# Kernel tuning notes

Measured on AMD Instinct MI355X. Metric: run time of the kernel, lower is better.

Reference implementation:

```python
import jax, jax.numpy as jnp
import numpy as np

WS = 7          # window size
SIZE = 56       # spatial H = W
SHIFT = 3       # shift_size = window_size // 2 (mask branch active)
NH = 4          # num heads
EPS = 1e-5


def _rel_pos_index(ws=WS):
    coords = np.stack(np.meshgrid(np.arange(ws), np.arange(ws), indexing='ij'))  # [2,ws,ws]
    coords = coords.reshape(2, -1)                               # [2, ws*ws]
    rel = coords[:, :, None] - coords[:, None, :]                # [2, N, N]
    rel = rel.transpose(1, 2, 0)                                 # [N, N, 2]
    rel[:, :, 0] += ws - 1
    rel[:, :, 1] += ws - 1
    rel[:, :, 0] *= 2 * ws - 1
    return jnp.asarray(rel[:, :, 0] + rel[:, :, 1])              # [N, N] int


def _attn_mask(size=SIZE, ws=WS, shift=SHIFT):
    img = np.zeros((size, size), dtype=np.float32)
    slices = (slice(0, -ws), slice(-ws, -shift), slice(-shift, None))
    cnt = 0
    for h in slices:
        for w in slices:
            img[h, w] = cnt
            cnt += 1
    nw = size // ws
    win = img.reshape(nw, ws, nw, ws).transpose(0, 2, 1, 3).reshape(-1, ws * ws)  # [nW, N]
    diff = win[:, None, :] - win[:, :, None]                    # [nW, N, N]
    mask = np.where(diff != 0, -100.0, 0.0).astype(np.float32)
    return jnp.asarray(mask)


def _layernorm(x, w, b):
    mu = jnp.mean(x, axis=-1, keepdims=True)
    var = jnp.mean(jnp.square(x - mu), axis=-1, keepdims=True)
    return (x - mu) * jax.lax.rsqrt(var + EPS) * w + b


def setup_inputs() -> dict:
    key = jax.random.key(0)
    ks = jax.random.split(key, 8)
    dim, dff = 128, 512
    s = lambda fan: 1.0 / np.sqrt(fan)
    return {
        'x': jax.random.normal(ks[0], (32, SIZE * SIZE, dim), jnp.float32),
        'qkv_w': jax.random.normal(ks[1], (dim, 3 * dim), jnp.float32) * s(dim),
        'qkv_b': jnp.zeros((3 * dim,), jnp.float32),
        'proj_w': jax.random.normal(ks[2], (dim, dim), jnp.float32) * s(dim),
        'proj_b': jnp.zeros((dim,), jnp.float32),
        'rpb_table': jax.random.normal(ks[3], ((2 * WS - 1) ** 2, NH), jnp.float32) * 0.02,
        'ln1_w': jnp.ones((dim,), jnp.float32),
        'ln1_b': jnp.zeros((dim,), jnp.float32),
        'ln2_w': jnp.ones((dim,), jnp.float32),
        'ln2_b': jnp.zeros((dim,), jnp.float32),
        'mlp_w1': jax.random.normal(ks[4], (dim, dff), jnp.float32) * s(dim),
        'mlp_b1': jnp.zeros((dff,), jnp.float32),
        'mlp_w2': jax.random.normal(ks[5], (dff, dim), jnp.float32) * s(dff),
        'mlp_b2': jnp.zeros((dim,), jnp.float32),
    }


def reference(x, qkv_w, qkv_b, proj_w, proj_b, rpb_table,
              ln1_w, ln1_b, ln2_w, ln2_b, mlp_w1, mlp_b1, mlp_w2, mlp_b2):
    B, L, C = x.shape
    N = WS * WS
    nw = SIZE // WS
    nW = nw * nw
    hd = C // NH
    scale = hd ** -0.5

    shortcut = x
    h = _layernorm(x, ln1_w, ln1_b).reshape(B, SIZE, SIZE, C)
    # window partition -> [B*nW, N, C]
    h = h.reshape(B, nw, WS, nw, WS, C).transpose(0, 1, 3, 2, 4, 5).reshape(B * nW, N, C)

    qkv = (h @ qkv_w + qkv_b).reshape(B * nW, N, 3, NH, hd)
    q, k, v = jnp.moveaxis(qkv, 2, 0)                 # each [B*nW, N, NH, hd]
    attn = jnp.einsum('bnhd,bmhd->bhnm', q * scale, k)  # [B*nW, NH, N, N]

    bias = rpb_table[_rel_pos_index()]                # [N, N, NH]
    attn = attn + bias.transpose(2, 0, 1)[None]

    mask = _attn_mask()                               # [nW, N, N]
    attn = attn.reshape(B, nW, NH, N, N) + mask[None, :, None]
    attn = jax.nn.softmax(attn.reshape(B * nW, NH, N, N), axis=-1)

    h = jnp.einsum('bhnm,bmhd->bnhd', attn, v).reshape(B * nW, N, C)
    h = h @ proj_w + proj_b

    # window reverse -> [B, L, C]
    h = h.reshape(B, nw, nw, WS, WS, C).transpose(0, 1, 3, 2, 4, 5).reshape(B, L, C)
    x = shortcut + h

    m = _layernorm(x, ln2_w, ln2_b)
    m = jax.nn.gelu(m @ mlp_w1 + mlp_b1, approximate=False) @ mlp_w2 + mlp_b2
    return x + m
```

## Files before the change

kernel.cpp:

```cpp
#include <hip/hip_runtime.h>
#include <hip/hip_bf16.h>

#define T_TOK   100352
#define NWIN    2048
#define EPS_LN  1e-5f

typedef __attribute__((ext_vector_type(8))) short bf16x8;
typedef __attribute__((ext_vector_type(4))) float f32x4;

__device__ inline unsigned short f2bf(float f) {
  union { float f; unsigned int i; } c; c.f = f;
  unsigned int x = c.i;
  x += 0x7fffu + ((x >> 16) & 1u);
  return (unsigned short)(x >> 16);
}
__device__ inline bf16x8 ld8(const unsigned short* p) {
  return *reinterpret_cast<const bf16x8*>(p);
}

__device__ inline int win_row_to_token(int r) {
  int win = r / 49, n = r % 49;
  int b  = win >> 6, w2 = win & 63;
  int wi = w2 >> 3,  wj = w2 & 7;
  int rr = n / 7,    cc = n % 7;
  return b * 3136 + (wi * 7 + rr) * 56 + (wj * 7 + cc);
}

__global__ void prep_weights(const float* __restrict__ qkv_w,
                             const float* __restrict__ proj_w,
                             const float* __restrict__ w1,
                             const float* __restrict__ w2,
                             unsigned short* __restrict__ wts) {
  int i = blockIdx.x * 256 + threadIdx.x;
  unsigned short* qkvt  = wts;
  unsigned short* projt = wts + 49152;
  unsigned short* w1t   = wts + 65536;
  unsigned short* w2t   = wts + 131072;
  if (i < 49152) {
    int n = i >> 7, k = i & 127; qkvt[i] = f2bf(qkv_w[k * 384 + n]);
  } else if (i < 65536) {
    int e = i - 49152; int n = e >> 7, k = e & 127; projt[e] = f2bf(proj_w[k * 128 + n]);
  } else if (i < 131072) {
    int e = i - 65536; int n = e >> 7, k = e & 127; w1t[e] = f2bf(w1[k * 512 + n]);
  } else if (i < 196608) {
    int e = i - 131072; int n = e >> 9, k = e & 511; w2t[e] = f2bf(w2[k * 128 + n]);
  }
}

__global__ void prep_cls(const float* __restrict__ rpb, float* __restrict__ cls2) {
  int i = blockIdx.x * 256 + threadIdx.x;
  int reg = i & 3, lane = (i >> 2) & 63, ct = (i >> 8) & 3, rt = (i >> 10) & 3,
      h = (i >> 12) & 3, cl = (i >> 14) & 3;
  int n = rt * 16 + ((lane >> 4) << 2) + reg;
  int m = ct * 16 + (lane & 15);
  float v = -30000.f;
  if (n < 49 && m < 49) {
    int nr = n / 7, nc = n % 7, mr = m / 7, mc = m % 7;
    v = rpb[((nr - mr + 6) * 13 + (nc - mc + 6)) * 4 + h];
    int regn = ((cl & 2) ? (nr < 4 ? 3 : 6) : 0) + ((cl & 1) ? (nc < 4 ? 1 : 2) : 0);
    int regm = ((cl & 2) ? (mr < 4 ? 3 : 6) : 0) + ((cl & 1) ? (mc < 4 ? 1 : 2) : 0);
    if (regn != regm) v -= 100.f;
  }
  cls2[i] = v;
}

template<bool WINMAP>
__global__ __launch_bounds__(256) void ln_kernel(const float* __restrict__ x,
                                                 const float* __restrict__ w,
                                                 const float* __restrict__ b,
                                                 unsigned short* __restrict__ out) {
  int r    = blockIdx.x * 4 + (threadIdx.x >> 6);
  int lane = threadIdx.x & 63;
  int src  = WINMAP ? win_row_to_token(r) : r;
  float2 v = *reinterpret_cast<const float2*>(x + (long)src * 128 + lane * 2);
  float s  = v.x + v.y;
  float s2 = v.x * v.x + v.y * v.y;
#pragma unroll
  for (int off = 32; off; off >>= 1) {
    s  += __shfl_xor(s,  off);
    s2 += __shfl_xor(s2, off);
  }
  float mu  = s * (1.f / 128.f);
  float var = s2 * (1.f / 128.f) - mu * mu;
  float inv = rsqrtf(var + EPS_LN);
  int c = lane * 2;
  float2 wv = *reinterpret_cast<const float2*>(w + c);
  float2 bv = *reinterpret_cast<const float2*>(b + c);
  float y0 = (v.x - mu) * inv * wv.x + bv.x;
  float y1 = (v.y - mu) * inv * wv.y + bv.y;
  unsigned int pk = ((unsigned int)f2bf(y1) << 16) | (unsigned int)f2bf(y0);
  *reinterpret_cast<unsigned int*>(out + (long)r * 128 + c) = pk;
}

template<int EPI, int KSTEPS, int NBN>
__global__ __launch_bounds__(256) void gemm_k(const unsigned short* __restrict__ A,
                                              const unsigned short* __restrict__ Wt,
                                              const float* __restrict__ bias,
                                              void* __restrict__ out,
                                              const float* __restrict__ res) {
  const int K = KSTEPS * 32;
  int flat  = blockIdx.x;
  int chunk = gridDim.x >> 3;
  int swz   = (flat & 7) * chunk + (flat >> 3);
  int ntile = swz % NBN, mpan = swz / NBN;

  int lane = threadIdx.x & 63;
  int wid  = threadIdx.x >> 6;
  int rowBase = mpan * 128 + wid * 32;
  int colBase = ntile * 64;
  int m  = lane & 15;
  int kg = lane >> 4;
  f32x4 acc[2][4] = {};
  const unsigned short* Ap = A  + (long)(rowBase + m) * K + kg * 8;
  const unsigned short* Bp = Wt + (long)(colBase + m) * K + kg * 8;
#pragma unroll 4
  for (int ks = 0; ks < KSTEPS; ks++) {
    bf16x8 b0 = ld8(Bp + 0 * 16 * K + ks * 32);
    bf16x8 b1 = ld8(Bp + 1 * 16 * K + ks * 32);
    bf16x8 b2 = ld8(Bp + 2 * 16 * K + ks * 32);
    bf16x8 b3 = ld8(Bp + 3 * 16 * K + ks * 32);
    bf16x8 a0 = ld8(Ap + ks * 32);
    bf16x8 a1 = ld8(Ap + (long)16 * K + ks * 32);
    acc[0][0] = __builtin_amdgcn_mfma_f32_16x16x32_bf16(a0, b0, acc[0][0], 0, 0, 0);
    acc[0][1] = __builtin_amdgcn_mfma_f32_16x16x32_bf16(a0, b1, acc[0][1], 0, 0, 0);
    acc[0][2] = __builtin_amdgcn_mfma_f32_16x16x32_bf16(a0, b2, acc[0][2], 0, 0, 0);
    acc[0][3] = __builtin_amdgcn_mfma_f32_16x16x32_bf16(a0, b3, acc[0][3], 0, 0, 0);
    acc[1][0] = __builtin_amdgcn_mfma_f32_16x16x32_bf16(a1, b0, acc[1][0], 0, 0, 0);
    acc[1][1] = __builtin_amdgcn_mfma_f32_16x16x32_bf16(a1, b1, acc[1][1], 0, 0, 0);
    acc[1][2] = __builtin_amdgcn_mfma_f32_16x16x32_bf16(a1, b2, acc[1][2], 0, 0, 0);
    acc[1][3] = __builtin_amdgcn_mfma_f32_16x16x32_bf16(a1, b3, acc[1][3], 0, 0, 0);
  }
#pragma unroll
  for (int mt = 0; mt < 2; mt++) {
#pragma unroll
    for (int rgi = 0; rgi < 4; rgi++) {
      int row = rowBase + mt * 16 + kg * 4 + rgi;
      int t = (EPI == 1) ? win_row_to_token(row) : row;
#pragma unroll
      for (int j = 0; j < 4; j++) {
        int col = colBase + j * 16 + m;
        float v = acc[mt][j][rgi] + bias[col];
        if (EPI == 0) {
          ((unsigned short*)out)[(long)row * 384 + col] = f2bf(v);
        } else {
          ((float*)out)[(long)t * 128 + col] = res[(long)t * 128 + col] + v;
        }
      }
    }
  }
}

__global__ __launch_bounds__(256) void attn_mfma(const unsigned short* __restrict__ qkv,
                                                 const float* __restrict__ cls2,
                                                 unsigned short* __restrict__ out) {
  __shared__ unsigned short vt[128 * 64];
  __shared__ unsigned short pb[4][64 * 64];
  int win = blockIdx.x;
  int tid = threadIdx.x;
  const unsigned short* qbase = qkv + (long)win * 49 * 384;

  for (int i = tid; i < 49 * 128; i += 256) {
    int mm = i >> 7, d = i & 127;
    vt[d * 64 + (mm ^ ((d & 7) << 3))] = qbase[mm * 384 + 256 + d];
  }
  for (int i = tid; i < 128 * 15; i += 256) {
    int d = i / 15, mm = 49 + i % 15;
    vt[d * 64 + (mm ^ ((d & 7) << 3))] = 0;
  }

  int h = tid >> 6, lane = tid & 63;
  int lr = lane & 15, g = lane >> 4;
  int w2 = win & 63;
  int cl = (((w2 >> 3) == 7) ? 2 : 0) + (((w2 & 7) == 7) ? 1 : 0);

  bf16x8 aq[4], bk[4];
  bf16x8 zf = {};
#pragma unroll
  for (int rt = 0; rt < 4; rt++)
    aq[rt] = ld8(qbase + (rt * 16 + lr) * 384 + h * 32 + g * 8);
#pragma unroll
  for (int ct = 0; ct < 4; ct++) {
    int mm = ct * 16 + lr;
    bk[ct] = (mm < 49) ? ld8(qbase + mm * 384 + 128 + h * 32 + g * 8) : zf;
  }
  f32x4 acc[4][4] = {};
#pragma unroll
  for (int rt = 0; rt < 4; rt++)
#pragma unroll
    for (int ct = 0; ct < 4; ct++)
      acc[rt][ct] = __builtin_amdgcn_mfma_f32_16x16x32_bf16(aq[rt], bk[ct], acc[rt][ct], 0, 0, 0);

  const float scale = 0.17677669529663687f;
  const float* cb = cls2 + (long)(cl * 4 + h) * 16 * 256;
  unsigned short* P = pb[h];
#pragma unroll
  for (int rt = 0; rt < 4; rt++) {
    f32x4 c[4];
#pragma unroll
    for (int ct = 0; ct < 4; ct++)
      c[ct] = *reinterpret_cast<const f32x4*>(cb + (rt * 4 + ct) * 256 + lane * 4);
#pragma unroll
    for (int reg = 0; reg < 4; reg++) {
      float s0 = acc[rt][0][reg] * scale + c[0][reg];
      float s1 = acc[rt][1][reg] * scale + c[1][reg];
      float s2 = acc[rt][2][reg] * scale + c[2][reg];
      float s3 = acc[rt][3][reg] * scale + c[3][reg];
      float mx = fmaxf(fmaxf(s0, s1), fmaxf(s2, s3));
      mx = fmaxf(mx, __shfl_xor(mx, 1)); mx = fmaxf(mx, __shfl_xor(mx, 2));
      mx = fmaxf(mx, __shfl_xor(mx, 4)); mx = fmaxf(mx, __shfl_xor(mx, 8));
      float p0 = __expf(s0 - mx), p1 = __expf(s1 - mx);
      float p2 = __expf(s2 - mx), p3 = __expf(s3 - mx);
      float sum = p0 + p1 + p2 + p3;
      sum += __shfl_xor(sum, 1); sum += __shfl_xor(sum, 2);
      sum += __shfl_xor(sum, 4); sum += __shfl_xor(sum, 8);
      float inv = 1.f / sum;
      int n = rt * 16 + g * 4 + reg;
      int sw = (n & 7) << 3, rowb = n * 64;
      P[rowb + ((0 * 16 + lr) ^ sw)] = f2bf(p0 * inv);
      P[rowb + ((1 * 16 + lr) ^ sw)] = f2bf(p1 * inv);
      P[rowb + ((2 * 16 + lr) ^ sw)] = f2bf(p2 * inv);
      P[rowb + ((3 * 16 + lr) ^ sw)] = f2bf(p3 * inv);
    }
  }
  __syncthreads();

  f32x4 o[4][2] = {};
  bf16x8 bv[2][2];
#pragma unroll
  for (int dt = 0; dt < 2; dt++)
#pragma unroll
    for (int ks = 0; ks < 2; ks++) {
      int d = h * 32 + dt * 16 + lr;
      bv[dt][ks] = ld8(&vt[d * 64 + ((ks * 32 + g * 8) ^ ((d & 7) << 3))]);
    }
#pragma unroll
  for (int rt = 0; rt < 4; rt++)
#pragma unroll
    for (int ks = 0; ks < 2; ks++) {
      int n = rt * 16 + lr;
      bf16x8 ap = ld8(&P[n * 64 + ((ks * 32 + g * 8) ^ ((n & 7) << 3))]);
#pragma unroll
      for (int dt = 0; dt < 2; dt++)
        o[rt][dt] = __builtin_amdgcn_mfma_f32_16x16x32_bf16(ap, bv[dt][ks], o[rt][dt], 0, 0, 0);
    }
#pragma unroll
  for (int rt = 0; rt < 4; rt++)
#pragma unroll
    for (int dt = 0; dt < 2; dt++)
#pragma unroll
      for (int reg = 0; reg < 4; reg++) {
        int n = rt * 16 + g * 4 + reg;
        if (n < 49)
          out[((long)win * 49 + n) * 128 + h * 32 + dt * 16 + lr] = f2bf(o[rt][dt][reg]);
      }
}

__global__ __launch_bounds__(512, 1) void mlp_fused(
    const float* __restrict__ out1,
    const unsigned short* __restrict__ w1t,
    const float* __restrict__ b1,
    const unsigned short* __restrict__ w2t,
    const float* __restrict__ b2,
    const float* __restrict__ ln2w,
    const float* __restrict__ ln2b,
    float* __restrict__ dout) {
  __shared__ unsigned short lnm[64 * 136];
  __shared__ unsigned short gel[64 * 520];
  long rowbase = (long)blockIdx.x * 64;
  int tid = threadIdx.x, w = tid >> 6, lane = tid & 63, lr = lane & 15, g = lane >> 4;

  {
    int c = lane * 2;
    float2 wv = *(const float2*)(ln2w + c);
    float2 bv = *(const float2*)(ln2b + c);
    for (int n = w; n < 64; n += 8) {
      float2 v = *(const float2*)(out1 + (rowbase + n) * 128 + c);
      float s = v.x + v.y, s2 = v.x * v.x + v.y * v.y;
#pragma unroll
      for (int off = 32; off; off >>= 1) { s += __shfl_xor(s, off); s2 += __shfl_xor(s2, off); }
      float mu  = s * (1.f / 128.f);
      float inv = rsqrtf(s2 * (1.f / 128.f) - mu * mu + EPS_LN);
      float y0 = (v.x - mu) * inv * wv.x + bv.x;
      float y1 = (v.y - mu) * inv * wv.y + bv.y;
      unsigned int pk = ((unsigned int)f2bf(y1) << 16) | f2bf(y0);
      *(unsigned int*)(lnm + n * 136 + c) = pk;
    }
  }
  __syncthreads();

  f32x4 acc[4][4] = {};
#pragma unroll
  for (int ksi = 0; ksi < 4; ksi++) {
    int kof = ksi * 32 + g * 8;
    bf16x8 av[4], bv[4];
#pragma unroll
    for (int rt = 0; rt < 4; rt++)
      av[rt] = ld8(lnm + (rt * 16 + lr) * 136 + kof);
#pragma unroll
    for (int ct = 0; ct < 4; ct++) {
      int colc = w * 64 + ct * 16 + lr;
      bv[ct] = ld8(w1t + colc * 128 + kof);
    }
#pragma unroll
    for (int rt = 0; rt < 4; rt++)
#pragma unroll
      for (int ct = 0; ct < 4; ct++)
        acc[rt][ct] = __builtin_amdgcn_mfma_f32_16x16x32_bf16(av[rt], bv[ct], acc[rt][ct], 0, 0, 0);
  }
#pragma unroll
  for (int ct = 0; ct < 4; ct++) {
    int c = w * 64 + ct * 16 + lr;
    float bc = b1[c];
#pragma unroll
    for (int rt = 0; rt < 4; rt++)
#pragma unroll
      for (int rgi = 0; rgi < 4; rgi++) {
        int n = rt * 16 + g * 4 + rgi;
        float v = acc[rt][ct][rgi] + bc;
        float u = v * (1.0f + 0.044715f * v * v);
        float gv = v / (1.0f + __expf(-1.5957691216f * u));
        gel[n * 520 + c] = f2bf(gv);
      }
  }
  __syncthreads();

  f32x4 a2[4] = {};
#pragma unroll 4
  for (int ksi = 0; ksi < 16; ksi++) {
    int kof = ksi * 32 + g * 8;
    bf16x8 aa[4];
#pragma unroll
    for (int rt = 0; rt < 4; rt++)
      aa[rt] = ld8(gel + (rt * 16 + lr) * 520 + kof);
    bf16x8 bb = ld8(w2t + (w * 16 + lr) * 512 + kof);
#pragma unroll
    for (int rt = 0; rt < 4; rt++)
      a2[rt] = __builtin_amdgcn_mfma_f32_16x16x32_bf16(aa[rt], bb, a2[rt], 0, 0, 0);
  }
  int col = w * 16 + lr;
  float bc2 = b2[col];
#pragma unroll
  for (int rt = 0; rt < 4; rt++)
#pragma unroll
    for (int rgi = 0; rgi < 4; rgi++) {
      long row = rowbase + rt * 16 + g * 4 + rgi;
      dout[row * 128 + col] = out1[row * 128 + col] + bc2 + a2[rt][rgi];
    }
}

extern "C" void kernel_launch(void* const* d_in, const int* in_sizes, int n_in,
                              void* d_out, int out_size, void* d_ws, size_t ws_size,
                              hipStream_t stream) {
  (void)in_sizes; (void)n_in; (void)out_size; (void)ws_size;
  const float* x      = (const float*)d_in[0];
  const float* qkv_w  = (const float*)d_in[1];
  const float* qkv_b  = (const float*)d_in[2];
  const float* proj_w = (const float*)d_in[3];
  const float* proj_b = (const float*)d_in[4];
  const float* rpb    = (const float*)d_in[5];
  const float* ln1_w  = (const float*)d_in[6];
  const float* ln1_b  = (const float*)d_in[7];
  const float* ln2_w  = (const float*)d_in[8];
  const float* ln2_b  = (const float*)d_in[9];
  const float* w1     = (const float*)d_in[10];
  const float* b1     = (const float*)d_in[11];
  const float* w2     = (const float*)d_in[12];
  const float* b2     = (const float*)d_in[13];

  char* ws = (char*)d_ws;
  unsigned short* wts   = (unsigned short*)ws;
  unsigned short* hb    = (unsigned short*)(ws + 393216);
  unsigned short* qkv   = (unsigned short*)(ws + 26083328);
  unsigned short* attno = hb;
  float*          out1  = (float*)(ws + 103153664);
  float*          cls2  = (float*)(ws + 154533888);

  const int MP = T_TOK / 128;

  prep_weights<<<768, 256, 0, stream>>>(qkv_w, proj_w, w1, w2, wts);
  prep_cls<<<256, 256, 0, stream>>>(rpb, cls2);
  ln_kernel<true><<<T_TOK / 4, 256, 0, stream>>>(x, ln1_w, ln1_b, hb);
  gemm_k<0, 4, 6><<<MP * 6, 256, 0, stream>>>(hb, wts, qkv_b, qkv, nullptr);
  attn_mfma<<<NWIN, 256, 0, stream>>>(qkv, cls2, attno);
  gemm_k<1, 4, 2><<<MP * 2, 256, 0, stream>>>(attno, wts + 49152, proj_b, out1, x);
  mlp_fused<<<T_TOK / 64, 512, 0, stream>>>(out1, wts + 65536, b1, wts + 131072, b2,
                                            ln2_w, ln2_b, (float*)d_out);
}
```

Before: 279.4 us.

## Vectorize QKV epilogue via swapped MFMA operands and fuse LN2 into MLP A-loads

For the QKV GEMM (EPI 0), the MFMA operands are swapped so each lane holds 4 consecutive output columns. The bias add and bf16 store can then be done as 4-wide vector accesses instead of scalar stores. In the MLP kernel, the LN2 shared-memory staging buffer and its barrier are removed: each lane computes row statistics with cross-group shuffles and normalizes its own fragments directly from global memory. The launch bound is also raised to allow more blocks per CU, at the cost of reading out1 twice from global/cache and possible register pressure.

```diff
diff --git a/kernel.cpp b/kernel.cpp
--- a/kernel.cpp
+++ b/kernel.cpp
@@ -7,6 +7,7 @@
 
 typedef __attribute__((ext_vector_type(8))) short bf16x8;
 typedef __attribute__((ext_vector_type(4))) float f32x4;
+typedef __attribute__((ext_vector_type(4))) unsigned short u16x4;
 
 __device__ inline unsigned short f2bf(float f) {
   union { float f; unsigned int i; } c; c.f = f;
@@ -115,34 +116,46 @@
   const unsigned short* Bp = Wt + (long)(colBase + m) * K + kg * 8;
 #pragma unroll 4
   for (int ks = 0; ks < KSTEPS; ks++) {
-    bf16x8 b0 = ld8(Bp + 0 * 16 * K + ks * 32);
-    bf16x8 b1 = ld8(Bp + 1 * 16 * K + ks * 32);
-    bf16x8 b2 = ld8(Bp + 2 * 16 * K + ks * 32);
-    bf16x8 b3 = ld8(Bp + 3 * 16 * K + ks * 32);
-    bf16x8 a0 = ld8(Ap + ks * 32);
-    bf16x8 a1 = ld8(Ap + (long)16 * K + ks * 32);
-    acc[0][0] = __builtin_amdgcn_mfma_f32_16x16x32_bf16(a0, b0, acc[0][0], 0, 0, 0);
-    acc[0][1] = __builtin_amdgcn_mfma_f32_16x16x32_bf16(a0, b1, acc[0][1], 0, 0, 0);
-    acc[0][2] = __builtin_amdgcn_mfma_f32_16x16x32_bf16(a0, b2, acc[0][2], 0, 0, 0);
-    acc[0][3] = __builtin_amdgcn_mfma_f32_16x16x32_bf16(a0, b3, acc[0][3], 0, 0, 0);
-    acc[1][0] = __builtin_amdgcn_mfma_f32_16x16x32_bf16(a1, b0, acc[1][0], 0, 0, 0);
-    acc[1][1] = __builtin_amdgcn_mfma_f32_16x16x32_bf16(a1, b1, acc[1][1], 0, 0, 0);
-    acc[1][2] = __builtin_amdgcn_mfma_f32_16x16x32_bf16(a1, b2, acc[1][2], 0, 0, 0);
-    acc[1][3] = __builtin_amdgcn_mfma_f32_16x16x32_bf16(a1, b3, acc[1][3], 0, 0, 0);
-  }
-#pragma unroll
-  for (int mt = 0; mt < 2; mt++) {
-#pragma unroll
-    for (int rgi = 0; rgi < 4; rgi++) {
-      int row = rowBase + mt * 16 + kg * 4 + rgi;
-      int t = (EPI == 1) ? win_row_to_token(row) : row;
+    bf16x8 bb[4], aa[2];
+#pragma unroll
+    for (int j = 0; j < 4; j++) bb[j] = ld8(Bp + (long)j * 16 * K + ks * 32);
+    aa[0] = ld8(Ap + ks * 32);
+    aa[1] = ld8(Ap + (long)16 * K + ks * 32);
+#pragma unroll
+    for (int mt = 0; mt < 2; mt++)
 #pragma unroll
       for (int j = 0; j < 4; j++) {
-        int col = colBase + j * 16 + m;
-        float v = acc[mt][j][rgi] + bias[col];
-        if (EPI == 0) {
-          ((unsigned short*)out)[(long)row * 384 + col] = f2bf(v);
-        } else {
+        if (EPI == 0)
+          acc[mt][j] = __builtin_amdgcn_mfma_f32_16x16x32_bf16(bb[j], aa[mt], acc[mt][j], 0, 0, 0);
+        else
+          acc[mt][j] = __builtin_amdgcn_mfma_f32_16x16x32_bf16(aa[mt], bb[j], acc[mt][j], 0, 0, 0);
+      }
+  }
+  if (EPI == 0) {
+#pragma unroll
+    for (int mt = 0; mt < 2; mt++) {
+      long trow = rowBase + mt * 16 + m;
+#pragma unroll
+      for (int j = 0; j < 4; j++) {
+        int wc = colBase + j * 16 + kg * 4;
+        f32x4 b4 = *reinterpret_cast<const f32x4*>(bias + wc);
+        u16x4 st;
+#pragma unroll
+        for (int rgi = 0; rgi < 4; rgi++) st[rgi] = f2bf(acc[mt][j][rgi] + b4[rgi]);
+        *reinterpret_cast<u16x4*>((unsigned short*)out + trow * 384 + wc) = st;
+      }
+    }
+  } else {
+#pragma unroll
+    for (int mt = 0; mt < 2; mt++) {
+#pragma unroll
+      for (int rgi = 0; rgi < 4; rgi++) {
+        int row = rowBase + mt * 16 + kg * 4 + rgi;
+        int t = win_row_to_token(row);
+#pragma unroll
+        for (int j = 0; j < 4; j++) {
+          int col = colBase + j * 16 + m;
+          float v = acc[mt][j][rgi] + bias[col];
           ((float*)out)[(long)t * 128 + col] = res[(long)t * 128 + col] + v;
         }
       }
@@ -255,7 +268,7 @@
       }
 }
 
-__global__ __launch_bounds__(512, 1) void mlp_fused(
+__global__ __launch_bounds__(512, 4) void mlp_fused(
     const float* __restrict__ out1,
     const unsigned short* __restrict__ w1t,
     const float* __restrict__ b1,
@@ -264,49 +277,65 @@
     const float* __restrict__ ln2w,
     const float* __restrict__ ln2b,
     float* __restrict__ dout) {
-  __shared__ unsigned short lnm[64 * 136];
   __shared__ unsigned short gel[64 * 520];
   long rowbase = (long)blockIdx.x * 64;
   int tid = threadIdx.x, w = tid >> 6, lane = tid & 63, lr = lane & 15, g = lane >> 4;
 
-  {
-    int c = lane * 2;
-    float2 wv = *(const float2*)(ln2w + c);
-    float2 bv = *(const float2*)(ln2b + c);
-    for (int n = w; n < 64; n += 8) {
-      float2 v = *(const float2*)(out1 + (rowbase + n) * 128 + c);
-      float s = v.x + v.y, s2 = v.x * v.x + v.y * v.y;
-#pragma unroll
-      for (int off = 32; off; off >>= 1) { s += __shfl_xor(s, off); s2 += __shfl_xor(s2, off); }
-      float mu  = s * (1.f / 128.f);
-      float inv = rsqrtf(s2 * (1.f / 128.f) - mu * mu + EPS_LN);
-      float y0 = (v.x - mu) * inv * wv.x + bv.x;
-      float y1 = (v.y - mu) * inv * wv.y + bv.y;
-      unsigned int pk = ((unsigned int)f2bf(y1) << 16) | f2bf(y0);
-      *(unsigned int*)(lnm + n * 136 + c) = pk;
-    }
-  }
-  __syncthreads();
+  float mu[4], inv[4];
+#pragma unroll
+  for (int rt = 0; rt < 4; rt++) {
+    const float* xr = out1 + (rowbase + rt * 16 + lr) * 128;
+    float s = 0.f, s2 = 0.f;
+#pragma unroll
+    for (int ksi = 0; ksi < 4; ksi++) {
+      f32x4 v0 = *(const f32x4*)(xr + ksi * 32 + g * 8);
+      f32x4 v1 = *(const f32x4*)(xr + ksi * 32 + g * 8 + 4);
+#pragma unroll
+      for (int j = 0; j < 4; j++) {
+        s  += v0[j] + v1[j];
+        s2 += v0[j] * v0[j] + v1[j] * v1[j];
+      }
+    }
+    s  += __shfl_xor(s, 16);  s  += __shfl_xor(s, 32);
+    s2 += __shfl_xor(s2, 16); s2 += __shfl_xor(s2, 32);
+    mu[rt]  = s * (1.f / 128.f);
+    inv[rt] = rsqrtf(s2 * (1.f / 128.f) - mu[rt] * mu[rt] + EPS_LN);
+  }
 
   f32x4 acc[4][4] = {};
 #pragma unroll
   for (int ksi = 0; ksi < 4; ksi++) {
     int kof = ksi * 32 + g * 8;
-    bf16x8 av[4], bv[4];
-#pragma unroll
-    for (int rt = 0; rt < 4; rt++)
-      av[rt] = ld8(lnm + (rt * 16 + lr) * 136 + kof);
-#pragma unroll
-    for (int ct = 0; ct < 4; ct++) {
-      int colc = w * 64 + ct * 16 + lr;
-      bv[ct] = ld8(w1t + colc * 128 + kof);
-    }
+    f32x4 lw0 = *(const f32x4*)(ln2w + kof), lw1 = *(const f32x4*)(ln2w + kof + 4);
+    f32x4 lb0 = *(const f32x4*)(ln2b + kof), lb1 = *(const f32x4*)(ln2b + kof + 4);
+    bf16x8 av[4];
+#pragma unroll
+    for (int rt = 0; rt < 4; rt++) {
+      const float* xr = out1 + (rowbase + rt * 16 + lr) * 128 + kof;
+      f32x4 v0 = *(const f32x4*)xr, v1 = *(const f32x4*)(xr + 4);
+      float e[8];
+#pragma unroll
+      for (int j = 0; j < 4; j++) {
+        e[j]     = (v0[j] - mu[rt]) * inv[rt] * lw0[j] + lb0[j];
+        e[4 + j] = (v1[j] - mu[rt]) * inv[rt] * lw1[j] + lb1[j];
+      }
+      union { unsigned int u[4]; bf16x8 v; } U;
+#pragma unroll
+      for (int d = 0; d < 4; d++)
+        U.u[d] = ((unsigned int)f2bf(e[2 * d + 1]) << 16) | (unsigned int)f2bf(e[2 * d]);
+      av[rt] = U.v;
+    }
+    bf16x8 bv[4];
+#pragma unroll
+    for (int ct = 0; ct < 4; ct++)
+      bv[ct] = ld8(w1t + (long)(w * 64 + ct * 16 + lr) * 128 + kof);
 #pragma unroll
     for (int rt = 0; rt < 4; rt++)
 #pragma unroll
       for (int ct = 0; ct < 4; ct++)
         acc[rt][ct] = __builtin_amdgcn_mfma_f32_16x16x32_bf16(av[rt], bv[ct], acc[rt][ct], 0, 0, 0);
   }
+
 #pragma unroll
   for (int ct = 0; ct < 4; ct++) {
     int c = w * 64 + ct * 16 + lr;
@@ -332,7 +361,7 @@
 #pragma unroll
     for (int rt = 0; rt < 4; rt++)
       aa[rt] = ld8(gel + (rt * 16 + lr) * 520 + kof);
-    bf16x8 bb = ld8(w2t + (w * 16 + lr) * 512 + kof);
+    bf16x8 bb = ld8(w2t + (long)(w * 16 + lr) * 512 + kof);
 #pragma unroll
     for (int rt = 0; rt < 4; rt++)
       a2[rt] = __builtin_amdgcn_mfma_f32_16x16x32_bf16(aa[rt], bb, a2[rt], 0, 0, 0);
```

After: 433.2 us. 1.55x slower.
